# Kernel optimization log

Measured on AMD Instinct MI355X. Metric: run time of the kernel, lower is better.

The kernel has to match this reference:

```python
import jax, jax.numpy as jnp
import numpy as np

ROPE_THETA = 10000.0

def _rope(t):
    # t: (B, S, H, D) -- rotate-half RoPE over last dim
    B, S, H, D = t.shape
    inv_freq = 1.0 / (ROPE_THETA ** (jnp.arange(0, D, 2, dtype=jnp.float32) / D))  # (D/2,)
    ang = jnp.arange(S, dtype=jnp.float32)[:, None] * inv_freq[None, :]            # (S, D/2)
    cos = jnp.concatenate([jnp.cos(ang), jnp.cos(ang)], axis=-1)[None, :, None, :] # (1,S,1,D)
    sin = jnp.concatenate([jnp.sin(ang), jnp.sin(ang)], axis=-1)[None, :, None, :]
    t1, t2 = jnp.split(t, 2, axis=-1)
    rot = jnp.concatenate([-t2, t1], axis=-1)
    return t * cos.astype(t.dtype) + rot * sin.astype(t.dtype)

def setup_inputs() -> dict:
    key = jax.random.key(0)
    kx, kq, kk, kv, ko = jax.random.split(key, 5)
    B, S, DIM = 2, 2048, 2048
    x = jax.random.normal(kx, (B, S, DIM), dtype=jnp.float32)
    mask = jnp.tril(jnp.ones((S, S), dtype=bool))[None, None, :, :]  # causal (1,1,S,S)
    scale = DIM ** -0.5
    wq = jax.random.normal(kq, (DIM, DIM), dtype=jnp.float32) * scale
    wk = jax.random.normal(kk, (DIM, DIM), dtype=jnp.float32) * scale
    wv = jax.random.normal(kv, (DIM, DIM), dtype=jnp.float32) * scale
    wo = jax.random.normal(ko, (DIM, DIM), dtype=jnp.float32) * scale
    return {"x": x, "mask": mask, "wq": wq, "wk": wk, "wv": wv, "wo": wo}

def reference(x, mask, wq, wk, wv, wo):
    B, S, DIM = x.shape
    H = 16
    D = DIM // H
    scale = D ** -0.5
    # nn.Linear: y = x @ W.T
    q = (x @ wq.T).reshape(B, S, H, D)
    k = (x @ wk.T).reshape(B, S, H, D)
    v = (x @ wv.T).reshape(B, S, H, D)
    q = _rope(q)
    k = _rope(k)
    scores = jnp.einsum('bqhd,bkhd->bhqk', q, k) * scale
    scores = jnp.where(mask, scores, -jnp.inf)
    attn = jax.nn.softmax(scores, axis=-1)
    out = jnp.einsum('bhqk,bkhd->bqhd', attn, v).reshape(B, S, DIM)
    return out @ wo.T
```

## Files before the change

### kernel.cpp

```cpp
#include <hip/hip_runtime.h>
#include <cstdint>

typedef unsigned short u16;
typedef uint32_t u32;
typedef __attribute__((ext_vector_type(8))) short bf16x8;
typedef __attribute__((ext_vector_type(4))) float f32x4;
typedef __attribute__((ext_vector_type(16))) float f32x16;

#define DIM_ 2048
#define S_   2048
#define B_   2
#define H_   16
#define HD_  128
#define M_   (B_ * S_)

__device__ __forceinline__ u16 f2b(float f) {
  union { float f; uint32_t u; } v; v.f = f;
  uint32_t u = v.u;
  return (u16)((u + 0x7FFFu + ((u >> 16) & 1u)) >> 16);
}
__device__ __forceinline__ float b2f(u16 h) {
  union { uint32_t u; float f; } v; v.u = ((uint32_t)h) << 16;
  return v.f;
}

__device__ __forceinline__ u32 cvtpk(float lo, float hi) {
  u32 r;
  asm("v_cvt_pk_bf16_f32 %0, %1, %2" : "=v"(r) : "v"(lo), "v"(hi));
  return r;
}

typedef __attribute__((address_space(3))) u16 lds_u16_t;
typedef __attribute__((address_space(1))) const u16 glob_u16_t;

__device__ __forceinline__ void gload16(const u16* g, u16* l) {
  __builtin_amdgcn_global_load_lds((glob_u16_t*)g, (lds_u16_t*)l, 16, 0, 0);
}
#define GLD0(SRC, DST) \
  __builtin_amdgcn_global_load_lds((glob_u16_t*)(SRC), (lds_u16_t*)(DST), 16, 0, 0)

__global__ void convert6_kernel(const float* __restrict__ x, const float* __restrict__ wq,
                                const float* __restrict__ wk, const float* __restrict__ wv,
                                const float* __restrict__ wo, u16* __restrict__ xb,
                                u16* __restrict__ wqb, u16* __restrict__ wkb,
                                u16* __restrict__ wvb, u16* __restrict__ wob,
                                float* __restrict__ cosT, float* __restrict__ sinT) {
  if (blockIdx.y == 5) {
    int idx = blockIdx.x * blockDim.x + threadIdx.x;
    if (idx >= 64 * S_) return;
    int d = idx >> 11;
    int s = idx & (S_ - 1);
    float inv = powf(10000.0f, -(float)d * (1.0f / 64.0f));
    float ang = (float)s * inv;
    cosT[idx] = cosf(ang);
    sinT[idx] = sinf(ang);
    return;
  }
  const float* src;
  u16* dst;
  int n;
  switch (blockIdx.y) {
    case 0: src = x;  dst = xb;  n = M_ * DIM_;   break;
    case 1: src = wq; dst = wqb; n = DIM_ * DIM_; break;
    case 2: src = wk; dst = wkb; n = DIM_ * DIM_; break;
    case 3: src = wv; dst = wvb; n = DIM_ * DIM_; break;
    default: src = wo; dst = wob; n = DIM_ * DIM_; break;
  }
  int i = (blockIdx.x * blockDim.x + threadIdx.x) * 4;
  const int stride = gridDim.x * blockDim.x * 4;
  for (; i < n; i += stride) {
    float4 v = *reinterpret_cast<const float4*>(src + i);
    uint64_t p = (uint64_t)f2b(v.x) | ((uint64_t)f2b(v.y) << 16) |
                 ((uint64_t)f2b(v.z) << 32) | ((uint64_t)f2b(v.w) << 48);
    *reinterpret_cast<uint64_t*>(dst + i) = p;
  }
}

#define NT_ 32

#define LDA(DST, BASE)                                                         \
  _Pragma("unroll") for (int mi = 0; mi < 8; ++mi)                             \
      DST[mi] = *(const bf16x8*)((BASE) + mi * 1024);
#define LDB(DST, BASE)                                                         \
  _Pragma("unroll") for (int ni = 0; ni < NF_; ++ni)                           \
      DST[ni] = *(const bf16x8*)((BASE) +                                      \
          (BPERM_ ? (((ni) & 1) * 1024 + ((ni) >> 1) * 4096) : (ni) * 1024));

#define MFMA_KS(AV, BV)                                                        \
  _Pragma("unroll") for (int mi = 0; mi < 8; ++mi)                             \
    _Pragma("unroll") for (int ni = 0; ni < NF_; ++ni)                         \
        acc[mi][ni] = __builtin_amdgcn_mfma_f32_16x16x32_bf16(                 \
            AV[mi], BV[ni], acc[mi][ni], 0, 0, 0);

#define STAGE(BUF, OFFU) do {                                                  \
    _Pragma("unroll") for (int s = 0; s < ASW_; ++s)                           \
      GLD0(sA + goff + (OFFU) + s * (64 * DIM_),                               \
           lds + (BUF) * BUFSZ_ + s * 4096 + w * 512);                         \
    _Pragma("unroll") for (int s = 0; s < BSW_; ++s)                           \
      GLD0(sB + goff + (OFFU) + s * (64 * DIM_),                               \
           lds + (BUF) * BUFSZ_ + 16384 + s * 4096 + w * 512);                 \
  } while (0)

#define VMC_N() do {                                                           \
    if (ASW_ + BSW_ == 8) asm volatile("s_waitcnt vmcnt(8)" ::: "memory");     \
    else                  asm volatile("s_waitcnt vmcnt(6)" ::: "memory");     \
  } while (0)

#define TILE_N(BUF, NBUF, OFFU) do {                                           \
    LDA(a1, pAk1[BUF]); LDB(b1, pBk1[BUF]);                            \
    __builtin_amdgcn_sched_barrier(0);                                         \
    __builtin_amdgcn_s_setprio(1);                                             \
    MFMA_KS(a0, b0);                                                  \
    __builtin_amdgcn_s_setprio(0);                                             \
    asm volatile("s_waitcnt lgkmcnt(0)" ::: "memory");                         \
    __builtin_amdgcn_sched_barrier(0);                                         \
    __builtin_amdgcn_s_barrier();                                      \
    STAGE(BUF, OFFU);                                                          \
    __builtin_amdgcn_sched_barrier(0);                                         \
    VMC_N();                                                                   \
    __builtin_amdgcn_sched_barrier(0);                                         \
    __builtin_amdgcn_s_barrier();                                      \
    LDA(a0, pAk0[NBUF]); LDB(b0, pBk0[NBUF]);                          \
    __builtin_amdgcn_sched_barrier(0);                                         \
    __builtin_amdgcn_s_setprio(1);                                             \
    MFMA_KS(a1, b1);                                                  \
    __builtin_amdgcn_s_setprio(0);                                             \
  } while (0)

#define TILE_P(BUF, NBUF) do {                                   \
    LDA(a1, pAk1[BUF]); LDB(b1, pBk1[BUF]);                                    \
    __builtin_amdgcn_sched_barrier(0);                                         \
    __builtin_amdgcn_s_setprio(1);                                             \
    MFMA_KS(a0, b0);                                                           \
    __builtin_amdgcn_s_setprio(0);                                             \
    asm volatile("s_waitcnt lgkmcnt(0)" ::: "memory");                         \
    __builtin_amdgcn_sched_barrier(0);                                         \
    asm volatile("s_waitcnt vmcnt(0)" ::: "memory");                           \
    __builtin_amdgcn_sched_barrier(0);                                         \
    __builtin_amdgcn_s_barrier();                                              \
    LDA(a0, pAk0[NBUF]); LDB(b0, pBk0[NBUF]);                                  \
    __builtin_amdgcn_sched_barrier(0);                                         \
    __builtin_amdgcn_s_setprio(1);                                             \
    MFMA_KS(a1, b1);                                                           \
    __builtin_amdgcn_s_setprio(0);                                             \
  } while (0)

#define TILE_L(BUF) do {                                         \
    LDA(a1, pAk1[BUF]); LDB(b1, pBk1[BUF]);                                    \
    __builtin_amdgcn_sched_barrier(0);                                         \
    MFMA_KS(a0, b0);                                                           \
    MFMA_KS(a1, b1);                                                           \
  } while (0)

#define GEMM_V2_BODY(BN_, BPERM__)                                             \
  constexpr int NF_ = (BN_) / 64;                                              \
  constexpr int BPERM_ = (BPERM__);                                            \
  constexpr int ASW_ = 4;                                                      \
  constexpr int BSW_ = (BN_) / 64;                                             \
  constexpr int BUFSZ_ = 16384 + (BN_) * 64;                                   \
  const int tid = threadIdx.x;                                                 \
  const int lane = tid & 63;                                                   \
  const int w = tid >> 6;                                                      \
  const int wm = w >> 2, wn = w & 3;                                           \
  const int l15 = lane & 15, lg = lane >> 4;                                   \
  const int goff = (w * 8 + (lane >> 3)) * DIM_ + ((lane & 7) ^ (lane >> 3)) * 8; \
  const int x7 = l15 & 7;                                                      \
  const int lr0 = l15 * 64 + ((lg ^ x7) * 8);                                  \
  const int lr1 = l15 * 64 + (((4 | lg) ^ x7) * 8);                            \
  const int bbase = BPERM_ ? ((wn >> 1) * 8192 + (wn & 1) * 2048)              \
                           : (wn * ((BN_) * 16));                              \
  const u16* pAk0[2] = {lds + wm * 8192 + lr0, lds + BUFSZ_ + wm * 8192 + lr0};\
  const u16* pAk1[2] = {lds + wm * 8192 + lr1, lds + BUFSZ_ + wm * 8192 + lr1};\
  const u16* pBk0[2] = {lds + 16384 + bbase + lr0,                             \
                        lds + BUFSZ_ + 16384 + bbase + lr0};                   \
  const u16* pBk1[2] = {lds + 16384 + bbase + lr1,                             \
                        lds + BUFSZ_ + 16384 + bbase + lr1};                   \
  f32x4 acc[8][NF_];                                                           \
  _Pragma("unroll") for (int i = 0; i < 8; ++i)                                \
    _Pragma("unroll") for (int j = 0; j < NF_; ++j)                            \
        acc[i][j] = (f32x4){0.f, 0.f, 0.f, 0.f};                               \
  bf16x8 a0[8], a1[8], b0[NF_], b1[NF_];                                       \
  STAGE(0, 0);                                                                 \
  STAGE(1, 64);                                                                \
  __builtin_amdgcn_sched_barrier(0);                                           \
  VMC_N();                                                                     \
  __builtin_amdgcn_sched_barrier(0);                                           \
  __builtin_amdgcn_s_barrier();                                                \
  LDA(a0, pAk0[0]); LDB(b0, pBk0[0]);                                          \
  for (int t = 0; t < NT_ - 2; t += 2) {                                       \
    TILE_N(0, 1, 128);                                                         \
    TILE_N(1, 0, 192);                                                         \
    sA += 128; sB += 128;                                                      \
  }                                                                            \
  TILE_P(0, 1);                                                                \
  TILE_L(1);

__global__ __launch_bounds__(512, 2) void gemm256_qkv_kernel(
    const u16* __restrict__ xb, const u16* __restrict__ wqb, const u16* __restrict__ wkb,
    const u16* __restrict__ wvb, u16* __restrict__ qb, u16* __restrict__ kb,
    u16* __restrict__ vtb, const float* __restrict__ cosT, const float* __restrict__ sinT) {
  __shared__ __align__(16) u16 lds[67584];

  const int bid = blockIdx.x;
  const int logical = (bid & 7) * 48 + (bid >> 3);
  const int mt = logical / 24;
  const int rem = logical % 24;
  const int z = rem >> 3;
  const int nt = rem & 7;
  const u16* Wm = (z == 0) ? wqb : (z == 1) ? wkb : wvb;
  u16* out = (z == 0) ? qb : (z == 1) ? kb : vtb;

  const u16* sA = xb + (size_t)(mt * 256) * DIM_;
  const u16* sB = Wm + (size_t)(nt * 256) * DIM_;

  GEMM_V2_BODY(256, 1)

  const int colbase = nt * 256 + (wn >> 1) * 128 + (wn & 1) * 32;
  if (z < 2) {
#pragma unroll
    for (int mi = 0; mi < 8; ++mi) {
      const int row = mt * 256 + wm * 128 + mi * 16 + lg * 4;
      const int s = row & (S_ - 1);
#pragma unroll
      for (int ni = 0; ni < 2; ++ni) {
        const int d = (wn & 1) * 32 + ni * 16 + l15;
        const float4 c4 = *(const float4*)(cosT + d * S_ + s);
        const float4 s4 = *(const float4*)(sinT + d * S_ + s);
        const float cc[4]  = {c4.x, c4.y, c4.z, c4.w};
        const float ssn[4] = {s4.x, s4.y, s4.z, s4.w};
        u16* p = out + (size_t)row * DIM_ + colbase + ni * 16 + l15;
#pragma unroll
        for (int r = 0; r < 4; ++r) {
          const float t1 = acc[mi][ni][r];
          const float t2 = acc[mi][ni + 2][r];
          p[(size_t)r * DIM_]      = f2b(t1 * cc[r] - t2 * ssn[r]);
          p[(size_t)r * DIM_ + 64] = f2b(t2 * cc[r] + t1 * ssn[r]);
        }
      }
    }
  } else {
    __builtin_amdgcn_s_barrier();
#pragma unroll
    for (int mi = 0; mi < 8; ++mi) {
      const int sl = wm * 128 + mi * 16 + lg * 4;
#pragma unroll
      for (int ni = 0; ni < 4; ++ni) {
        const int cl = (wn >> 1) * 128 + (wn & 1) * 32 + (ni & 1) * 16 + (ni >> 1) * 64 + l15;
        const u32 lo  = cvtpk(acc[mi][ni][0], acc[mi][ni][1]);
        const u32 hi2 = cvtpk(acc[mi][ni][2], acc[mi][ni][3]);
        const uint64_t pk = (uint64_t)lo | ((uint64_t)hi2 << 32);
        *(uint64_t*)(lds + cl * 264 + sl) = pk;
      }
    }
    __builtin_amdgcn_s_barrier();
    asm volatile("s_waitcnt lgkmcnt(0)" ::: "memory");
    const int l31_ = lane & 31;
    const int hi_ = lane >> 5;
    const int bq = (mt * 256) >> 11;
    const int sbase = (mt * 256) & (S_ - 1);
#pragma unroll
    for (int it = 0; it < 16; ++it) {
      const int d = it * 16 + w * 2 + hi_;
      const int colg = nt * 256 + d;
      const int hh = colg >> 7, dd = colg & 127;
      const bf16x8 val = *(const bf16x8*)(lds + d * 264 + l31_ * 8);
      *(bf16x8*)(out + ((size_t)(bq * 16 + hh) * 128 + dd) * S_ + sbase + l31_ * 8) = val;
    }
  }
}

__global__ __launch_bounds__(512, 2) void gemm_out_v2_kernel(const u16* __restrict__ A,
                                                             const u16* __restrict__ W,
                                                             float* __restrict__ Cf) {
  __shared__ __align__(16) u16 lds[49152];
  const int bid = blockIdx.x;
  const int logical = (bid & 7) * 32 + (bid >> 3);
  const int mt = logical >> 4;
  const int nt = logical & 15;

  const u16* sA = A + (size_t)(mt * 256) * DIM_;
  const u16* sB = W + (size_t)(nt * 128) * DIM_;

  GEMM_V2_BODY(128, 0)

#pragma unroll
  for (int mi = 0; mi < 8; ++mi)
#pragma unroll
    for (int ni = 0; ni < 2; ++ni) {
      const int row = mt * 256 + wm * 128 + mi * 16 + lg * 4;
      const int col = nt * 128 + wn * 32 + ni * 16 + l15;
#pragma unroll
      for (int r = 0; r < 4; ++r)
        Cf[(size_t)(row + r) * DIM_ + col] = acc[mi][ni][r];
    }
}

#define CEXP 0.12751744f

__global__ __launch_bounds__(256, 2) void attn_kernel(const u16* __restrict__ q,
                                                      const u16* __restrict__ k,
                                                      const u16* __restrict__ vt,
                                                      u16* __restrict__ ao) {
  __shared__ __align__(16) u16 smem[32768];
  u16* kTl = smem;
  u16* vTl = smem + 16384;

  const int qt   = blockIdx.z ? (int)blockIdx.x : (int)(gridDim.x - 1 - blockIdx.x);
  const int head = blockIdx.y;
  const int b    = blockIdx.z;
  const int t = threadIdx.x;
  const int lane = t & 63;
  const int w = t >> 6;
  const int l31 = lane & 31;
  const int hi = lane >> 5;
  const int kxor = (lane & 7) << 3;
  const int qrow0 = qt * 128 + w * 32;
  const size_t bS = (size_t)b * S_;
  const size_t vhead = (size_t)(b * 16 + head) * 128 * S_;

  bf16x8 qf[8];
  {
    const u16* qrow = q + (bS + qrow0 + l31) * DIM_ + head * HD_;
#pragma unroll
    for (int st = 0; st < 8; ++st)
      qf[st] = *(const bf16x8*)(qrow + st * 16 + hi * 8);
  }

  f32x16 accO[4];
#pragma unroll
  for (int db = 0; db < 4; ++db)
#pragma unroll
    for (int rr = 0; rr < 16; ++rr) accO[db][rr] = 0.f;
  float m = -1e30f, l = 0.f;

  const int tmax_w = 2 * qt + (w >> 1);
  const int ttend = 2 * qt + 1;

  auto stageK = [&](int buf, int tt) {
#pragma unroll
    for (int p = 0; p < 4; ++p) {
      const int cid = p * 256 + w * 64 + lane;
      const int kr = cid >> 4;
      const int cg = (cid & 15) ^ (kr & 7);
      gload16(k + (bS + tt * 64 + kr) * DIM_ + head * HD_ + cg * 8,
              kTl + buf * 8192 + (p * 256 + w * 64) * 8);
    }
  };
  auto stageV = [&](int buf, int tt) {
#pragma unroll
    for (int p = 0; p < 4; ++p) {
      const int cid = p * 256 + w * 64 + lane;
      const int d = cid >> 3;
      const int cg = (cid & 7) ^ (d & 7);
      gload16(vt + vhead + (size_t)d * S_ + tt * 64 + cg * 8,
              vTl + buf * 8192 + (p * 256 + w * 64) * 8);
    }
  };

  stageK(0, 0);
  stageV(0, 0);
  __syncthreads();

  for (int tt = 0; tt <= ttend; ++tt) {
    const int cur = tt & 1;
    const int alt = cur ^ 1;

    if (tt + 1 <= ttend) {
      stageK(alt, tt + 1);
      stageV(alt, tt + 1);
    }

    if (tt <= tmax_w) {
      const u16* kB = kTl + cur * 8192;
      const u16* vB = vTl + cur * 8192;
      f32x16 sA, sB;
#pragma unroll
      for (int rr = 0; rr < 16; ++rr) { sA[rr] = 0.f; sB[rr] = 0.f; }
      __builtin_amdgcn_s_setprio(1);
#pragma unroll
      for (int st = 0; st < 8; ++st) {
        const int dc = st * 16 + hi * 8;
        bf16x8 k0 = *(const bf16x8*)(kB + l31 * 128 + (dc ^ kxor));
        bf16x8 k1 = *(const bf16x8*)(kB + (32 + l31) * 128 + (dc ^ kxor));
        sA = __builtin_amdgcn_mfma_f32_32x32x16_bf16(k0, qf[st], sA, 0, 0, 0);
        sB = __builtin_amdgcn_mfma_f32_32x32x16_bf16(k1, qf[st], sB, 0, 0, 0);
      }
      __builtin_amdgcn_s_setprio(0);

      const int qg = qrow0 + l31;
      if (tt * 64 + 63 > qrow0) {
        const int kb = tt * 64 + 4 * hi;
#pragma unroll
        for (int rr = 0; rr < 16; ++rr) {
          const int kg = kb + (rr & 3) + 8 * (rr >> 2);
          sA[rr] = (kg <= qg) ? sA[rr] : -1e30f;
          sB[rr] = (kg + 32 <= qg) ? sB[rr] : -1e30f;
        }
      }

      float mx[8];
#pragma unroll
      for (int i = 0; i < 8; ++i)
        mx[i] = fmaxf(fmaxf(sA[i], sA[i + 8]), fmaxf(sB[i], sB[i + 8]));
#pragma unroll
      for (int i = 0; i < 4; ++i) mx[i] = fmaxf(mx[i], mx[i + 4]);
      float pm = fmaxf(fmaxf(mx[0], mx[1]), fmaxf(mx[2], mx[3]));
      pm = fmaxf(pm, __shfl_xor(pm, 32));
      const float mN = fmaxf(m, pm);
      if (!__all(pm - m <= 90.5f)) {
        const float osc = exp2f((m - mN) * CEXP);
        l *= osc;
#pragma unroll
        for (int db = 0; db < 4; ++db)
#pragma unroll
          for (int rr = 0; rr < 16; ++rr) accO[db][rr] *= osc;
        m = mN;
      }
      const float mc = m * CEXP;
      float lsv[4] = {0.f, 0.f, 0.f, 0.f};
#pragma unroll
      for (int rr = 0; rr < 16; ++rr) {
        const float pa = exp2f(__builtin_fmaf(sA[rr], CEXP, -mc));
        const float pb = exp2f(__builtin_fmaf(sB[rr], CEXP, -mc));
        sA[rr] = pa; sB[rr] = pb;
        lsv[rr & 3] += pa + pb;
      }
      float ls = (lsv[0] + lsv[1]) + (lsv[2] + lsv[3]);
      ls += __shfl_xor(ls, 32);
      l += ls;

#define PV_STEP(ARR, R0, ST2)                                                      \
      {                                                                            \
        u32 a0 = cvtpk(ARR[(R0) + 0], ARR[(R0) + 1]);                              \
        u32 a1 = cvtpk(ARR[(R0) + 2], ARR[(R0) + 3]);                              \
        u32 b0 = cvtpk(ARR[(R0) + 4], ARR[(R0) + 5]);                              \
        u32 b1 = cvtpk(ARR[(R0) + 6], ARR[(R0) + 7]);                              \
        asm("v_permlane32_swap_b32 %0, %1" : "+v"(a0), "+v"(b0));                  \
        asm("v_permlane32_swap_b32 %0, %1" : "+v"(a1), "+v"(b1));                  \
        union { u32 uu[4]; bf16x8 v8; } pf;                                        \
        pf.uu[0] = a0; pf.uu[1] = a1; pf.uu[2] = b0; pf.uu[3] = b1;                \
        const int ko = (ST2) * 16 + hi * 8;                                        \
        __builtin_amdgcn_s_setprio(1);                                             \
        _Pragma("unroll")                                                          \
        for (int db = 0; db < 4; ++db) {                                           \
          const int dr = db * 32 + l31;                                            \
          bf16x8 vf = *(const bf16x8*)(vB + dr * 64 + (ko ^ kxor));                \
          accO[db] =                                                               \
              __builtin_amdgcn_mfma_f32_32x32x16_bf16(vf, pf.v8, accO[db], 0, 0, 0); \
        }                                                                          \
        __builtin_amdgcn_s_setprio(0);                                             \
      }
      PV_STEP(sA, 0, 0)
      PV_STEP(sA, 8, 1)
      PV_STEP(sB, 0, 2)
      PV_STEP(sB, 8, 3)
#undef PV_STEP
    }

    __syncthreads();
  }

  const float linv = 1.0f / l;
  u16* oT = smem + w * 4352;
#pragma unroll
  for (int db = 0; db < 4; ++db)
#pragma unroll
    for (int q4 = 0; q4 < 4; ++q4) {
      const int dbase = db * 32 + q4 * 8 + hi * 4;
      const u32 lo = cvtpk(accO[db][q4 * 4 + 0] * linv, accO[db][q4 * 4 + 1] * linv);
      const u32 hiw = cvtpk(accO[db][q4 * 4 + 2] * linv, accO[db][q4 * 4 + 3] * linv);
      *(u32*)(oT + l31 * 136 + dbase) = lo;
      *(u32*)(oT + l31 * 136 + dbase + 2) = hiw;
    }
  __syncthreads();
#pragma unroll
  for (int i = 0; i < 8; ++i) {
    const int cid = i * 64 + lane;
    const int qloc = cid >> 4;
    const int c = cid & 15;
    const bf16x8 val = *(const bf16x8*)(oT + qloc * 136 + c * 8);
    *(bf16x8*)(ao + (bS + qrow0 + qloc) * DIM_ + head * HD_ + c * 8) = val;
  }
}

extern "C" void kernel_launch(void* const* d_in, const int* in_sizes, int n_in,
                              void* d_out, int out_size, void* d_ws, size_t ws_size,
                              hipStream_t stream) {
  const float* x  = (const float*)d_in[0];
  const float* wq = (const float*)d_in[2];
  const float* wk = (const float*)d_in[3];
  const float* wv = (const float*)d_in[4];
  const float* wo = (const float*)d_in[5];

  char* ws = (char*)d_ws;
  size_t off = 0;
  auto carve = [&](size_t bytes) { char* p = ws + off; off += bytes; return p; };
  u16* xb   = (u16*)carve((size_t)M_ * DIM_ * 2);
  u16* wqb  = (u16*)carve((size_t)DIM_ * DIM_ * 2);
  u16* wkb  = (u16*)carve((size_t)DIM_ * DIM_ * 2);
  u16* wvb  = (u16*)carve((size_t)DIM_ * DIM_ * 2);
  u16* wob  = (u16*)carve((size_t)DIM_ * DIM_ * 2);
  u16* qb   = (u16*)carve((size_t)M_ * DIM_ * 2);
  u16* kb   = (u16*)carve((size_t)M_ * DIM_ * 2);
  u16* vtb  = (u16*)carve((size_t)M_ * DIM_ * 2);
  u16* aob  = (u16*)carve((size_t)M_ * DIM_ * 2);
  float* cosT = (float*)carve((size_t)64 * S_ * 4);
  float* sinT = (float*)carve((size_t)64 * S_ * 4);
  if (off > ws_size) return;

  dim3 gc(1024, 6);
  convert6_kernel<<<gc, 256, 0, stream>>>(x, wq, wk, wv, wo, xb, wqb, wkb, wvb, wob,
                                          cosT, sinT);

  gemm256_qkv_kernel<<<384, 512, 0, stream>>>(xb, wqb, wkb, wvb, qb, kb, vtb, cosT, sinT);

  dim3 ga(16, H_, B_);
  attn_kernel<<<ga, 256, 0, stream>>>(qb, kb, vtb, aob);

  gemm_out_v2_kernel<<<256, 512, 0, stream>>>(aob, wob, (float*)d_out);
}
```

Baseline: 245.9 us.

## Replace double-buffered 256-wide GEMMs with smaller single-buffer tiles and higher occupancy

Both projection GEMMs drop the double-buffered, hand-scheduled pipeline macros for a simple single-buffer loop with smaller tiles. QKV moves from 256x256 to 256x128 tiles over 768 blocks, and the output GEMM from 256x128 to 128x128 tiles over 512 blocks with 256 threads. The aim is to cut LDS use and raise occupancy (launch bounds go to 4 blocks per CU) so other wavefronts hide global-load latency. The cost is losing explicit prefetch overlap, adding two syncthreads per k-step, and getting less reuse per tile; the V transpose epilogue is redone in two halves.

```diff
diff --git a/kernel.cpp b/kernel.cpp
--- a/kernel.cpp
+++ b/kernel.cpp
@@ -78,157 +78,99 @@
 
 #define NT_ 32
 
-#define LDA(DST, BASE)                                                         \
-  _Pragma("unroll") for (int mi = 0; mi < 8; ++mi)                             \
-      DST[mi] = *(const bf16x8*)((BASE) + mi * 1024);
-#define LDB(DST, BASE)                                                         \
-  _Pragma("unroll") for (int ni = 0; ni < NF_; ++ni)                           \
-      DST[ni] = *(const bf16x8*)((BASE) +                                      \
-          (BPERM_ ? (((ni) & 1) * 1024 + ((ni) >> 1) * 4096) : (ni) * 1024));
-
-#define MFMA_KS(AV, BV)                                                        \
-  _Pragma("unroll") for (int mi = 0; mi < 8; ++mi)                             \
-    _Pragma("unroll") for (int ni = 0; ni < NF_; ++ni)                         \
-        acc[mi][ni] = __builtin_amdgcn_mfma_f32_16x16x32_bf16(                 \
-            AV[mi], BV[ni], acc[mi][ni], 0, 0, 0);
-
-#define STAGE(BUF, OFFU) do {                                                  \
-    _Pragma("unroll") for (int s = 0; s < ASW_; ++s)                           \
-      GLD0(sA + goff + (OFFU) + s * (64 * DIM_),                               \
-           lds + (BUF) * BUFSZ_ + s * 4096 + w * 512);                         \
-    _Pragma("unroll") for (int s = 0; s < BSW_; ++s)                           \
-      GLD0(sB + goff + (OFFU) + s * (64 * DIM_),                               \
-           lds + (BUF) * BUFSZ_ + 16384 + s * 4096 + w * 512);                 \
-  } while (0)
-
-#define VMC_N() do {                                                           \
-    if (ASW_ + BSW_ == 8) asm volatile("s_waitcnt vmcnt(8)" ::: "memory");     \
-    else                  asm volatile("s_waitcnt vmcnt(6)" ::: "memory");     \
-  } while (0)
-
-#define TILE_N(BUF, NBUF, OFFU) do {                                           \
-    LDA(a1, pAk1[BUF]); LDB(b1, pBk1[BUF]);                            \
-    __builtin_amdgcn_sched_barrier(0);                                         \
-    __builtin_amdgcn_s_setprio(1);                                             \
-    MFMA_KS(a0, b0);                                                  \
-    __builtin_amdgcn_s_setprio(0);                                             \
-    asm volatile("s_waitcnt lgkmcnt(0)" ::: "memory");                         \
-    __builtin_amdgcn_sched_barrier(0);                                         \
-    __builtin_amdgcn_s_barrier();                                      \
-    STAGE(BUF, OFFU);                                                          \
-    __builtin_amdgcn_sched_barrier(0);                                         \
-    VMC_N();                                                                   \
-    __builtin_amdgcn_sched_barrier(0);                                         \
-    __builtin_amdgcn_s_barrier();                                      \
-    LDA(a0, pAk0[NBUF]); LDB(b0, pBk0[NBUF]);                          \
-    __builtin_amdgcn_sched_barrier(0);                                         \
-    __builtin_amdgcn_s_setprio(1);                                             \
-    MFMA_KS(a1, b1);                                                  \
-    __builtin_amdgcn_s_setprio(0);                                             \
-  } while (0)
-
-#define TILE_P(BUF, NBUF) do {                                   \
-    LDA(a1, pAk1[BUF]); LDB(b1, pBk1[BUF]);                                    \
-    __builtin_amdgcn_sched_barrier(0);                                         \
-    __builtin_amdgcn_s_setprio(1);                                             \
-    MFMA_KS(a0, b0);                                                           \
-    __builtin_amdgcn_s_setprio(0);                                             \
-    asm volatile("s_waitcnt lgkmcnt(0)" ::: "memory");                         \
-    __builtin_amdgcn_sched_barrier(0);                                         \
-    asm volatile("s_waitcnt vmcnt(0)" ::: "memory");                           \
-    __builtin_amdgcn_sched_barrier(0);                                         \
-    __builtin_amdgcn_s_barrier();                                              \
-    LDA(a0, pAk0[NBUF]); LDB(b0, pBk0[NBUF]);                                  \
-    __builtin_amdgcn_sched_barrier(0);                                         \
-    __builtin_amdgcn_s_setprio(1);                                             \
-    MFMA_KS(a1, b1);                                                           \
-    __builtin_amdgcn_s_setprio(0);                                             \
-  } while (0)
-
-#define TILE_L(BUF) do {                                         \
-    LDA(a1, pAk1[BUF]); LDB(b1, pBk1[BUF]);                                    \
-    __builtin_amdgcn_sched_barrier(0);                                         \
-    MFMA_KS(a0, b0);                                                           \
-    MFMA_KS(a1, b1);                                                           \
-  } while (0)
-
-#define GEMM_V2_BODY(BN_, BPERM__)                                             \
-  constexpr int NF_ = (BN_) / 64;                                              \
-  constexpr int BPERM_ = (BPERM__);                                            \
-  constexpr int ASW_ = 4;                                                      \
-  constexpr int BSW_ = (BN_) / 64;                                             \
-  constexpr int BUFSZ_ = 16384 + (BN_) * 64;                                   \
-  const int tid = threadIdx.x;                                                 \
-  const int lane = tid & 63;                                                   \
-  const int w = tid >> 6;                                                      \
-  const int wm = w >> 2, wn = w & 3;                                           \
-  const int l15 = lane & 15, lg = lane >> 4;                                   \
-  const int goff = (w * 8 + (lane >> 3)) * DIM_ + ((lane & 7) ^ (lane >> 3)) * 8; \
-  const int x7 = l15 & 7;                                                      \
-  const int lr0 = l15 * 64 + ((lg ^ x7) * 8);                                  \
-  const int lr1 = l15 * 64 + (((4 | lg) ^ x7) * 8);                            \
-  const int bbase = BPERM_ ? ((wn >> 1) * 8192 + (wn & 1) * 2048)              \
-                           : (wn * ((BN_) * 16));                              \
-  const u16* pAk0[2] = {lds + wm * 8192 + lr0, lds + BUFSZ_ + wm * 8192 + lr0};\
-  const u16* pAk1[2] = {lds + wm * 8192 + lr1, lds + BUFSZ_ + wm * 8192 + lr1};\
-  const u16* pBk0[2] = {lds + 16384 + bbase + lr0,                             \
-                        lds + BUFSZ_ + 16384 + bbase + lr0};                   \
-  const u16* pBk1[2] = {lds + 16384 + bbase + lr1,                             \
-                        lds + BUFSZ_ + 16384 + bbase + lr1};                   \
-  f32x4 acc[8][NF_];                                                           \
-  _Pragma("unroll") for (int i = 0; i < 8; ++i)                                \
-    _Pragma("unroll") for (int j = 0; j < NF_; ++j)                            \
-        acc[i][j] = (f32x4){0.f, 0.f, 0.f, 0.f};                               \
-  bf16x8 a0[8], a1[8], b0[NF_], b1[NF_];                                       \
-  STAGE(0, 0);                                                                 \
-  STAGE(1, 64);                                                                \
-  __builtin_amdgcn_sched_barrier(0);                                           \
-  VMC_N();                                                                     \
-  __builtin_amdgcn_sched_barrier(0);                                           \
-  __builtin_amdgcn_s_barrier();                                                \
-  LDA(a0, pAk0[0]); LDB(b0, pBk0[0]);                                          \
-  for (int t = 0; t < NT_ - 2; t += 2) {                                       \
-    TILE_N(0, 1, 128);                                                         \
-    TILE_N(1, 0, 192);                                                         \
-    sA += 128; sB += 128;                                                      \
-  }                                                                            \
-  TILE_P(0, 1);                                                                \
-  TILE_L(1);
-
-__global__ __launch_bounds__(512, 2) void gemm256_qkv_kernel(
+__global__ __launch_bounds__(512, 4) void gemm_qkv3_kernel(
     const u16* __restrict__ xb, const u16* __restrict__ wqb, const u16* __restrict__ wkb,
     const u16* __restrict__ wvb, u16* __restrict__ qb, u16* __restrict__ kb,
     u16* __restrict__ vtb, const float* __restrict__ cosT, const float* __restrict__ sinT) {
-  __shared__ __align__(16) u16 lds[67584];
+  __shared__ __align__(16) u16 lds[24576];
 
   const int bid = blockIdx.x;
-  const int logical = (bid & 7) * 48 + (bid >> 3);
-  const int mt = logical / 24;
-  const int rem = logical % 24;
-  const int z = rem >> 3;
-  const int nt = rem & 7;
+  const int logical = (bid & 7) * 96 + (bid >> 3);
+  const int mt = logical / 48;
+  const int rem = logical % 48;
+  const int z = rem >> 4;
+  const int nt = rem & 15;
   const u16* Wm = (z == 0) ? wqb : (z == 1) ? wkb : wvb;
   u16* out = (z == 0) ? qb : (z == 1) ? kb : vtb;
 
+  const int tid = threadIdx.x;
+  const int lane = tid & 63;
+  const int w = tid >> 6;
+  const int wm = w >> 1, wn = w & 1;
+  const int l15 = lane & 15, lg = lane >> 4;
+
   const u16* sA = xb + (size_t)(mt * 256) * DIM_;
-  const u16* sB = Wm + (size_t)(nt * 256) * DIM_;
-
-  GEMM_V2_BODY(256, 1)
-
-  const int colbase = nt * 256 + (wn >> 1) * 128 + (wn & 1) * 32;
+  const u16* sB = Wm + (size_t)(nt * 128) * DIM_;
+
+  const int r8 = tid >> 3;
+  const int goffs = r8 * DIM_ + (((tid & 7) ^ (r8 & 7)) * 8);
+
+  const int x7 = l15 & 7;
+  const int lrk0 = ((lg) ^ x7) * 8;
+  const int lrk1 = ((4 | lg) ^ x7) * 8;
+  const u16* pA0 = lds + (wm * 64 + l15) * 64 + lrk0;
+  const u16* pA1 = lds + (wm * 64 + l15) * 64 + lrk1;
+  const u16* pB0 = lds + 16384 + (wn * 32 + l15) * 64 + lrk0;
+  const u16* pB1 = lds + 16384 + (wn * 32 + l15) * 64 + lrk1;
+
+  f32x4 acc[4][4];
+#pragma unroll
+  for (int i = 0; i < 4; ++i)
+#pragma unroll
+    for (int j = 0; j < 4; ++j) acc[i][j] = (f32x4){0.f, 0.f, 0.f, 0.f};
+
+  bf16x8 a[4], b[4];
+
+  for (int t = 0; t < NT_; ++t) {
+    __syncthreads();
+#pragma unroll
+    for (int s = 0; s < 4; ++s)
+      GLD0(sA + goffs + s * (64 * DIM_), lds + s * 4096 + w * 512);
+#pragma unroll
+    for (int s = 0; s < 2; ++s)
+      GLD0(sB + goffs + s * (64 * DIM_), lds + 16384 + s * 4096 + w * 512);
+    sA += 64; sB += 64;
+    __syncthreads();
+
+#pragma unroll
+    for (int mi = 0; mi < 4; ++mi) a[mi] = *(const bf16x8*)(pA0 + mi * 1024);
+#pragma unroll
+    for (int ni = 0; ni < 4; ++ni)
+      b[ni] = *(const bf16x8*)(pB0 + (ni & 1) * 1024 + (ni >> 1) * 4096);
+    __builtin_amdgcn_s_setprio(1);
+#pragma unroll
+    for (int mi = 0; mi < 4; ++mi)
+#pragma unroll
+      for (int ni = 0; ni < 4; ++ni)
+        acc[mi][ni] = __builtin_amdgcn_mfma_f32_16x16x32_bf16(a[mi], b[ni], acc[mi][ni], 0, 0, 0);
+    __builtin_amdgcn_s_setprio(0);
+#pragma unroll
+    for (int mi = 0; mi < 4; ++mi) a[mi] = *(const bf16x8*)(pA1 + mi * 1024);
+#pragma unroll
+    for (int ni = 0; ni < 4; ++ni)
+      b[ni] = *(const bf16x8*)(pB1 + (ni & 1) * 1024 + (ni >> 1) * 4096);
+    __builtin_amdgcn_s_setprio(1);
+#pragma unroll
+    for (int mi = 0; mi < 4; ++mi)
+#pragma unroll
+      for (int ni = 0; ni < 4; ++ni)
+        acc[mi][ni] = __builtin_amdgcn_mfma_f32_16x16x32_bf16(a[mi], b[ni], acc[mi][ni], 0, 0, 0);
+    __builtin_amdgcn_s_setprio(0);
+  }
+
   if (z < 2) {
 #pragma unroll
-    for (int mi = 0; mi < 8; ++mi) {
-      const int row = mt * 256 + wm * 128 + mi * 16 + lg * 4;
+    for (int mi = 0; mi < 4; ++mi) {
+      const int row = mt * 256 + wm * 64 + mi * 16 + lg * 4;
       const int s = row & (S_ - 1);
 #pragma unroll
       for (int ni = 0; ni < 2; ++ni) {
-        const int d = (wn & 1) * 32 + ni * 16 + l15;
+        const int d = wn * 32 + ni * 16 + l15;
         const float4 c4 = *(const float4*)(cosT + d * S_ + s);
         const float4 s4 = *(const float4*)(sinT + d * S_ + s);
         const float cc[4]  = {c4.x, c4.y, c4.z, c4.w};
         const float ssn[4] = {s4.x, s4.y, s4.z, s4.w};
-        u16* p = out + (size_t)row * DIM_ + colbase + ni * 16 + l15;
+        u16* p = out + (size_t)row * DIM_ + nt * 128 + d;
 #pragma unroll
         for (int r = 0; r < 4; ++r) {
           const float t1 = acc[mi][ni][r];
@@ -239,56 +181,117 @@
       }
     }
   } else {
-    __builtin_amdgcn_s_barrier();
-#pragma unroll
-    for (int mi = 0; mi < 8; ++mi) {
-      const int sl = wm * 128 + mi * 16 + lg * 4;
-#pragma unroll
-      for (int ni = 0; ni < 4; ++ni) {
-        const int cl = (wn >> 1) * 128 + (wn & 1) * 32 + (ni & 1) * 16 + (ni >> 1) * 64 + l15;
-        const u32 lo  = cvtpk(acc[mi][ni][0], acc[mi][ni][1]);
-        const u32 hi2 = cvtpk(acc[mi][ni][2], acc[mi][ni][3]);
-        const uint64_t pk = (uint64_t)lo | ((uint64_t)hi2 << 32);
-        *(uint64_t*)(lds + cl * 264 + sl) = pk;
-      }
-    }
-    __builtin_amdgcn_s_barrier();
-    asm volatile("s_waitcnt lgkmcnt(0)" ::: "memory");
+    const int bq = mt >> 3;
+    const int sbase = (mt * 256) & (S_ - 1);
     const int l31_ = lane & 31;
-    const int hi_ = lane >> 5;
-    const int bq = (mt * 256) >> 11;
-    const int sbase = (mt * 256) & (S_ - 1);
-#pragma unroll
-    for (int it = 0; it < 16; ++it) {
-      const int d = it * 16 + w * 2 + hi_;
-      const int colg = nt * 256 + d;
-      const int hh = colg >> 7, dd = colg & 127;
-      const bf16x8 val = *(const bf16x8*)(lds + d * 264 + l31_ * 8);
-      *(bf16x8*)(out + ((size_t)(bq * 16 + hh) * 128 + dd) * S_ + sbase + l31_ * 8) = val;
-    }
-  }
-}
-
-__global__ __launch_bounds__(512, 2) void gemm_out_v2_kernel(const u16* __restrict__ A,
-                                                             const u16* __restrict__ W,
-                                                             float* __restrict__ Cf) {
-  __shared__ __align__(16) u16 lds[49152];
+    (void)l31_;
+#pragma unroll
+    for (int shalf = 0; shalf < 2; ++shalf) {
+      __syncthreads();
+      if ((wm >> 1) == shalf) {
+#pragma unroll
+        for (int mi = 0; mi < 4; ++mi) {
+          const int sl = (wm & 1) * 64 + mi * 16 + lg * 4;
+#pragma unroll
+          for (int ni = 0; ni < 4; ++ni) {
+            const int d = wn * 32 + (ni & 1) * 16 + (ni >> 1) * 64 + l15;
+            const u32 lo  = cvtpk(acc[mi][ni][0], acc[mi][ni][1]);
+            const u32 hi2 = cvtpk(acc[mi][ni][2], acc[mi][ni][3]);
+            const uint64_t pk = (uint64_t)lo | ((uint64_t)hi2 << 32);
+            *(uint64_t*)(lds + d * 136 + sl) = pk;
+          }
+        }
+      }
+      __syncthreads();
+#pragma unroll
+      for (int it = 0; it < 4; ++it) {
+        const int d = it * 32 + w * 4 + (lane >> 4);
+        const bf16x8 val = *(const bf16x8*)(lds + d * 136 + (lane & 15) * 8);
+        *(bf16x8*)(out + ((size_t)(bq * 16 + nt) * 128 + d) * S_ + sbase + shalf * 128 +
+                   (lane & 15) * 8) = val;
+      }
+    }
+  }
+}
+
+__global__ __launch_bounds__(256, 4) void gemm_out3_kernel(const u16* __restrict__ A,
+                                                           const u16* __restrict__ W,
+                                                           float* __restrict__ Cf) {
+  __shared__ __align__(16) u16 lds[16384];
   const int bid = blockIdx.x;
-  const int logical = (bid & 7) * 32 + (bid >> 3);
+  const int logical = (bid & 7) * 64 + (bid >> 3);
   const int mt = logical >> 4;
   const int nt = logical & 15;
 
-  const u16* sA = A + (size_t)(mt * 256) * DIM_;
+  const int tid = threadIdx.x;
+  const int lane = tid & 63;
+  const int w = tid >> 6;
+  const int wm = w >> 1, wn = w & 1;
+  const int l15 = lane & 15, lg = lane >> 4;
+
+  const u16* sA = A + (size_t)(mt * 128) * DIM_;
   const u16* sB = W + (size_t)(nt * 128) * DIM_;
 
-  GEMM_V2_BODY(128, 0)
-
-#pragma unroll
-  for (int mi = 0; mi < 8; ++mi)
-#pragma unroll
-    for (int ni = 0; ni < 2; ++ni) {
-      const int row = mt * 256 + wm * 128 + mi * 16 + lg * 4;
-      const int col = nt * 128 + wn * 32 + ni * 16 + l15;
+  const int r8 = tid >> 3;
+  const int goffs = r8 * DIM_ + (((tid & 7) ^ (r8 & 7)) * 8);
+
+  const int x7 = l15 & 7;
+  const int lrk0 = ((lg) ^ x7) * 8;
+  const int lrk1 = ((4 | lg) ^ x7) * 8;
+  const u16* pA0 = lds + (wm * 64 + l15) * 64 + lrk0;
+  const u16* pA1 = lds + (wm * 64 + l15) * 64 + lrk1;
+  const u16* pB0 = lds + 8192 + (wn * 64 + l15) * 64 + lrk0;
+  const u16* pB1 = lds + 8192 + (wn * 64 + l15) * 64 + lrk1;
+
+  f32x4 acc[4][4];
+#pragma unroll
+  for (int i = 0; i < 4; ++i)
+#pragma unroll
+    for (int j = 0; j < 4; ++j) acc[i][j] = (f32x4){0.f, 0.f, 0.f, 0.f};
+
+  bf16x8 a[4], b[4];
+
+  for (int t = 0; t < NT_; ++t) {
+    __syncthreads();
+#pragma unroll
+    for (int s = 0; s < 4; ++s)
+      GLD0(sA + goffs + s * (32 * DIM_), lds + s * 2048 + w * 512);
+#pragma unroll
+    for (int s = 0; s < 4; ++s)
+      GLD0(sB + goffs + s * (32 * DIM_), lds + 8192 + s * 2048 + w * 512);
+    sA += 64; sB += 64;
+    __syncthreads();
+
+#pragma unroll
+    for (int mi = 0; mi < 4; ++mi) a[mi] = *(const bf16x8*)(pA0 + mi * 1024);
+#pragma unroll
+    for (int ni = 0; ni < 4; ++ni) b[ni] = *(const bf16x8*)(pB0 + ni * 1024);
+    __builtin_amdgcn_s_setprio(1);
+#pragma unroll
+    for (int mi = 0; mi < 4; ++mi)
+#pragma unroll
+      for (int ni = 0; ni < 4; ++ni)
+        acc[mi][ni] = __builtin_amdgcn_mfma_f32_16x16x32_bf16(a[mi], b[ni], acc[mi][ni], 0, 0, 0);
+    __builtin_amdgcn_s_setprio(0);
+#pragma unroll
+    for (int mi = 0; mi < 4; ++mi) a[mi] = *(const bf16x8*)(pA1 + mi * 1024);
+#pragma unroll
+    for (int ni = 0; ni < 4; ++ni) b[ni] = *(const bf16x8*)(pB1 + ni * 1024);
+    __builtin_amdgcn_s_setprio(1);
+#pragma unroll
+    for (int mi = 0; mi < 4; ++mi)
+#pragma unroll
+      for (int ni = 0; ni < 4; ++ni)
+        acc[mi][ni] = __builtin_amdgcn_mfma_f32_16x16x32_bf16(a[mi], b[ni], acc[mi][ni], 0, 0, 0);
+    __builtin_amdgcn_s_setprio(0);
+  }
+
+#pragma unroll
+  for (int mi = 0; mi < 4; ++mi)
+#pragma unroll
+    for (int ni = 0; ni < 4; ++ni) {
+      const int row = mt * 128 + wm * 64 + mi * 16 + lg * 4;
+      const int col = nt * 128 + wn * 64 + ni * 16 + l15;
 #pragma unroll
       for (int r = 0; r < 4; ++r)
         Cf[(size_t)(row + r) * DIM_ + col] = acc[mi][ni][r];
@@ -512,10 +515,10 @@
   convert6_kernel<<<gc, 256, 0, stream>>>(x, wq, wk, wv, wo, xb, wqb, wkb, wvb, wob,
                                           cosT, sinT);
 
-  gemm256_qkv_kernel<<<384, 512, 0, stream>>>(xb, wqb, wkb, wvb, qb, kb, vtb, cosT, sinT);
+  gemm_qkv3_kernel<<<768, 512, 0, stream>>>(xb, wqb, wkb, wvb, qb, kb, vtb, cosT, sinT);
 
   dim3 ga(16, H_, B_);
   attn_kernel<<<ga, 256, 0, stream>>>(qb, kb, vtb, aob);
 
-  gemm_out_v2_kernel<<<256, 512, 0, stream>>>(aob, wob, (float*)d_out);
-}
+  gemm_out3_kernel<<<512, 256, 0, stream>>>(aob, wob, (float*)d_out);
+}
```

After: 241.5 us. About the same (-1.8%).
